# Performance work log

Measured on AMD Instinct MI355X. Metric: run time of the kernel, lower is better.

The kernel has to match this reference:

```python
import jax, jax.numpy as jnp
import numpy as np

CUTOFF = 5.0  # Angstrom contact cutoff for atom interaction mask
N, L, ATOMS, D, H = 1, 64, 14, 128, 64
M = L * ATOMS  # 896 atoms


def atom_interaction_mask_batch(pos14, ppi_code, cutoff=CUTOFF):
    # pos14: (N, L, 14, 3), ppi_code: (N, L) -> mask (N, L*14, L*14)
    n, l = ppi_code.shape
    pos = pos14.reshape(n, l * ATOMS, 3)
    d2 = jnp.sum((pos[:, :, None, :] - pos[:, None, :, :]) ** 2, axis=-1)  # (N,M,M)
    codes = jnp.repeat(ppi_code, ATOMS, axis=1)  # (N,M)
    cross_chain = codes[:, :, None] != codes[:, None, :]
    return (d2 < cutoff * cutoff) & cross_chain


def _edge_feats(feats, W1, b1, mask):
    # Decompose fc_1(concat(f_i, f_j)) = f_i @ W1[:, :D].T + f_j @ W1[:, D:].T + b1
    # so the (N,M,M,2D) concat tensor is never materialized.
    d = feats.shape[-1]
    hi = feats @ W1[:, :d].T  # (N,M,H)
    hj = feats @ W1[:, d:].T  # (N,M,H)
    e = hi[:, :, None, :] + hj[:, None, :, :] + b1  # (N,M,M,H)
    return jnp.where(mask[..., None], e, 0.0)


def setup_inputs() -> dict:
    key = jax.random.key(0)
    ks = jax.random.split(key, 8)
    feats_wt = jax.random.normal(ks[0], (N, M, D), dtype=jnp.float32)
    feats_mut = jax.random.normal(ks[1], (N, M, D), dtype=jnp.float32)
    # scale positions so the 5A cutoff yields a sparse, realistic contact mask
    pos14_wt = jax.random.normal(ks[2], (N, L, ATOMS, 3), dtype=jnp.float32) * 10.0
    pos14_mut = pos14_wt + jax.random.normal(ks[3], (N, L, ATOMS, 3), dtype=jnp.float32) * 0.5
    ppi_code_wt = jax.random.randint(ks[4], (N, L), 0, 2)
    ppi_code_mut = ppi_code_wt
    # fc_1: Linear(2D -> H), fc_2: Linear(H -> 1), torch layout W:(out,in)
    W1 = jax.random.normal(ks[5], (H, 2 * D), dtype=jnp.float32) / np.sqrt(2 * D)
    b1 = jnp.zeros((H,), dtype=jnp.float32)
    W2 = jax.random.normal(ks[6], (1, H), dtype=jnp.float32) / np.sqrt(H)
    b2 = jnp.zeros((1,), dtype=jnp.float32)
    return dict(feats_wt=feats_wt, feats_mut=feats_mut, pos14_wt=pos14_wt,
                pos14_mut=pos14_mut, ppi_code_wt=ppi_code_wt,
                ppi_code_mut=ppi_code_mut, W1=W1, b1=b1, W2=W2, b2=b2)


def reference(feats_wt, feats_mut, pos14_wt, pos14_mut, ppi_code_wt,
              ppi_code_mut, W1, b1, W2, b2):
    mask_wt = atom_interaction_mask_batch(pos14_wt, ppi_code_wt)
    mask_mut = atom_interaction_mask_batch(pos14_mut, ppi_code_mut)
    e_wt = _edge_feats(feats_wt, W1, b1, mask_wt)    # (N,M,M,H)
    e_mut = _edge_feats(feats_mut, W1, b1, mask_mut)  # (N,M,M,H)
    diff = e_mut - e_wt
    n = diff.shape[0]
    # (n, l1, 14, l2, 14, H) -> sum over residues l1, l2 -> (n, 14, 14, H)
    blocks = diff.reshape(n, L, ATOMS, L, ATOMS, H).sum(axis=(1, 3))
    out = blocks @ W2.T + b2  # (n,14,14,1)
    return out.reshape(n, -1)  # (n, 196)
```

## Files before the change

kernel.cpp:

```cpp
#include <hip/hip_runtime.h>

#define LRES   64
#define ATOMS  14
#define M      896
#define DF     128
#define HF     64
#define CUT2   25.0f

#define U_OFF    0
#define V_OFF    128
#define SB_OFF   256
#define SIW_OFF  320
#define SJW_OFF  (320 + 896)
#define SIM_OFF  (320 + 2*896)
#define SJM_OFF  (320 + 3*896)
#define PART_OFF (320 + 4*896)

__global__ void k_prep_uv(const float* __restrict__ W1, const float* __restrict__ b1,
                          const float* __restrict__ W2, float* __restrict__ ws) {
    int t = threadIdx.x;
    float s = 0.f;
    #pragma unroll
    for (int h = 0; h < HF; ++h) s += W2[h] * W1[h * (2 * DF) + t];
    ws[t] = s;
    if (t == 0) {
        float sb = 0.f;
        #pragma unroll
        for (int h = 0; h < HF; ++h) sb += W2[h] * b1[h];
        ws[SB_OFF] = sb;
    }
}

__global__ void k_prep_s(const float* __restrict__ feats_wt,
                         const float* __restrict__ feats_mut,
                         float* __restrict__ ws) {
    int i = blockIdx.x;
    int t = threadIdx.x;
    const float* u = ws + U_OFF;
    const float* v = ws + V_OFF;
    float fw0 = feats_wt[i * DF + t],  fw1 = feats_wt[i * DF + 64 + t];
    float fm0 = feats_mut[i * DF + t], fm1 = feats_mut[i * DF + 64 + t];
    float u0 = u[t], u1 = u[64 + t], v0 = v[t], v1 = v[64 + t];
    float siw = fw0 * u0 + fw1 * u1;
    float sjw = fw0 * v0 + fw1 * v1;
    float sim = fm0 * u0 + fm1 * u1;
    float sjm = fm0 * v0 + fm1 * v1;
    #pragma unroll
    for (int off = 32; off > 0; off >>= 1) {
        siw += __shfl_down(siw, off);
        sjw += __shfl_down(sjw, off);
        sim += __shfl_down(sim, off);
        sjm += __shfl_down(sjm, off);
    }
    if (t == 0) {
        ws[SIW_OFF + i] = siw;
        ws[SJW_OFF + i] = sjw;
        ws[SIM_OFF + i] = sim;
        ws[SJM_OFF + i] = sjm;
    }
}

__global__ void k_pairs(const float* __restrict__ pos_wt,
                        const float* __restrict__ pos_mut,
                        const int* __restrict__ ppi_wt,
                        const int* __restrict__ ppi_mut,
                        float* __restrict__ ws) {
    int i = blockIdx.x;
    int t = threadIdx.x;
    __shared__ float acc[16][14];

    float pwx = pos_wt[i * 3 + 0], pwy = pos_wt[i * 3 + 1], pwz = pos_wt[i * 3 + 2];
    float pmx = pos_mut[i * 3 + 0], pmy = pos_mut[i * 3 + 1], pmz = pos_mut[i * 3 + 2];
    int cw_i = ppi_wt[i / ATOMS];
    int cm_i = ppi_mut[i / ATOMS];
    float sb = ws[SB_OFF];
    float base_w = ws[SIW_OFF + i] + sb;
    float base_m = ws[SIM_OFF + i] + sb;
    const float* sjw = ws + SJW_OFF;
    const float* sjm = ws + SJM_OFF;

    if (t < 14 * 16) {
        int a2 = t % ATOMS;
        int k  = t / ATOMS;
        float c = 0.f;
        for (int l2 = k; l2 < LRES; l2 += 16) {
            int j = l2 * ATOMS + a2;
            if (ppi_wt[l2] != cw_i) {
                float dx = pwx - pos_wt[j * 3 + 0];
                float dy = pwy - pos_wt[j * 3 + 1];
                float dz = pwz - pos_wt[j * 3 + 2];
                float d2 = dx * dx + dy * dy + dz * dz;
                if (d2 < CUT2) c -= base_w + sjw[j];
            }
            if (ppi_mut[l2] != cm_i) {
                float dx = pmx - pos_mut[j * 3 + 0];
                float dy = pmy - pos_mut[j * 3 + 1];
                float dz = pmz - pos_mut[j * 3 + 2];
                float d2 = dx * dx + dy * dy + dz * dz;
                if (d2 < CUT2) c += base_m + sjm[j];
            }
        }
        acc[k][a2] = c;
    }
    __syncthreads();
    if (t < ATOMS) {
        float s = 0.f;
        #pragma unroll
        for (int k = 0; k < 16; ++k) s += acc[k][t];
        ws[PART_OFF + i * ATOMS + t] = s;
    }
}

__global__ void k_final(const float* __restrict__ b2, const float* __restrict__ ws,
                        float* __restrict__ out) {
    int t = threadIdx.x;
    if (t < ATOMS * ATOMS) {
        int a1 = t / ATOMS, a2 = t % ATOMS;
        float s = 0.f;
        #pragma unroll
        for (int l1 = 0; l1 < LRES; ++l1)
            s += ws[PART_OFF + (l1 * ATOMS + a1) * ATOMS + a2];
        out[t] = s + b2[0];
    }
}

extern "C" void kernel_launch(void* const* d_in, const int* in_sizes, int n_in,
                              void* d_out, int out_size, void* d_ws, size_t ws_size,
                              hipStream_t stream) {
    const float* feats_wt  = (const float*)d_in[0];
    const float* feats_mut = (const float*)d_in[1];
    const float* pos_wt    = (const float*)d_in[2];
    const float* pos_mut   = (const float*)d_in[3];
    const int*   ppi_wt    = (const int*)d_in[4];
    const int*   ppi_mut   = (const int*)d_in[5];
    const float* W1        = (const float*)d_in[6];
    const float* b1        = (const float*)d_in[7];
    const float* W2        = (const float*)d_in[8];
    const float* b2        = (const float*)d_in[9];
    float* out = (float*)d_out;
    float* ws  = (float*)d_ws;

    k_prep_uv<<<1, 256, 0, stream>>>(W1, b1, W2, ws);
    k_prep_s<<<M, 64, 0, stream>>>(feats_wt, feats_mut, ws);
    k_pairs<<<M, 256, 0, stream>>>(pos_wt, pos_mut, ppi_wt, ppi_mut, ws);
    k_final<<<1, 256, 0, stream>>>(b2, ws, out);
}
```

Before: 18.37 us.

## Fuse all four kernels into one per-output-block kernel using contact counts

Replaces the four-kernel pipeline (prep u/v, prep per-atom scalars, pair scan, final reduce) with a single kernel of 196 blocks, one per output atom pair (a1,a2). Each block recomputes the folded W2·W1 vectors in shared memory and, for each residue l1, counts cutoff-satisfying cross-chain contacts for the row atom and the column atom. It then multiplies those counts by per-atom projected features, so no workspace round trips or extra launches are needed. The cost is redundant recomputation of u/v and the feature dot products in every block, and fewer blocks (196) than before.

```diff
diff --git a/kernel.cpp b/kernel.cpp
--- a/kernel.cpp
+++ b/kernel.cpp
@@ -7,120 +7,112 @@
 #define HF     64
 #define CUT2   25.0f
 
-#define U_OFF    0
-#define V_OFF    128
-#define SB_OFF   256
-#define SIW_OFF  320
-#define SJW_OFF  (320 + 896)
-#define SIM_OFF  (320 + 2*896)
-#define SJM_OFF  (320 + 3*896)
-#define PART_OFF (320 + 4*896)
+__global__ __launch_bounds__(256) void k_fused(
+    const float* __restrict__ feats_wt, const float* __restrict__ feats_mut,
+    const float* __restrict__ pos_wt,   const float* __restrict__ pos_mut,
+    const int* __restrict__ ppi_wt,     const int* __restrict__ ppi_mut,
+    const float* __restrict__ W1, const float* __restrict__ b1,
+    const float* __restrict__ W2, const float* __restrict__ b2,
+    float* __restrict__ out)
+{
+    const int b  = blockIdx.x;
+    const int a1 = b / ATOMS, a2 = b % ATOMS;
+    const int t  = threadIdx.x;
+    const int l1 = t >> 2;
+    const int c  = t & 3;
 
-__global__ void k_prep_uv(const float* __restrict__ W1, const float* __restrict__ b1,
-                          const float* __restrict__ W2, float* __restrict__ ws) {
-    int t = threadIdx.x;
-    float s = 0.f;
-    #pragma unroll
-    for (int h = 0; h < HF; ++h) s += W2[h] * W1[h * (2 * DF) + t];
-    ws[t] = s;
-    if (t == 0) {
-        float sb = 0.f;
-        #pragma unroll
-        for (int h = 0; h < HF; ++h) sb += W2[h] * b1[h];
-        ws[SB_OFF] = sb;
-    }
-}
+    __shared__ float u[DF], v[DF];
+    __shared__ float sbs;
+    __shared__ float part[LRES];
 
-__global__ void k_prep_s(const float* __restrict__ feats_wt,
-                         const float* __restrict__ feats_mut,
-                         float* __restrict__ ws) {
-    int i = blockIdx.x;
-    int t = threadIdx.x;
-    const float* u = ws + U_OFF;
-    const float* v = ws + V_OFF;
-    float fw0 = feats_wt[i * DF + t],  fw1 = feats_wt[i * DF + 64 + t];
-    float fm0 = feats_mut[i * DF + t], fm1 = feats_mut[i * DF + 64 + t];
-    float u0 = u[t], u1 = u[64 + t], v0 = v[t], v1 = v[64 + t];
-    float siw = fw0 * u0 + fw1 * u1;
-    float sjw = fw0 * v0 + fw1 * v1;
-    float sim = fm0 * u0 + fm1 * u1;
-    float sjm = fm0 * v0 + fm1 * v1;
-    #pragma unroll
-    for (int off = 32; off > 0; off >>= 1) {
-        siw += __shfl_down(siw, off);
-        sjw += __shfl_down(sjw, off);
-        sim += __shfl_down(sim, off);
-        sjm += __shfl_down(sjm, off);
+    {
+        const int d = t & 127;
+        const float* col = W1 + ((t < 128) ? d : (DF + d));
+        float s = 0.f;
+        #pragma unroll 8
+        for (int h = 0; h < HF; ++h) s += W2[h] * col[h * (2 * DF)];
+        if (t < 128) u[d] = s; else v[d] = s;
     }
     if (t == 0) {
-        ws[SIW_OFF + i] = siw;
-        ws[SJW_OFF + i] = sjw;
-        ws[SIM_OFF + i] = sim;
-        ws[SJM_OFF + i] = sjm;
+        float s = 0.f;
+        #pragma unroll
+        for (int h = 0; h < HF; ++h) s += W2[h] * b1[h];
+        sbs = s;
     }
-}
 
-__global__ void k_pairs(const float* __restrict__ pos_wt,
-                        const float* __restrict__ pos_mut,
-                        const int* __restrict__ ppi_wt,
-                        const int* __restrict__ ppi_mut,
-                        float* __restrict__ ws) {
-    int i = blockIdx.x;
-    int t = threadIdx.x;
-    __shared__ float acc[16][14];
+    const int i_row = l1 * ATOMS + a1;
+    const int j_col = l1 * ATOMS + a2;
+    const float rwx = pos_wt [i_row*3], rwy = pos_wt [i_row*3+1], rwz = pos_wt [i_row*3+2];
+    const float rmx = pos_mut[i_row*3], rmy = pos_mut[i_row*3+1], rmz = pos_mut[i_row*3+2];
+    const float cwx = pos_wt [j_col*3], cwy = pos_wt [j_col*3+1], cwz = pos_wt [j_col*3+2];
+    const float cmx = pos_mut[j_col*3], cmy = pos_mut[j_col*3+1], cmz = pos_mut[j_col*3+2];
+    const int codew = ppi_wt[l1], codem = ppi_mut[l1];
 
-    float pwx = pos_wt[i * 3 + 0], pwy = pos_wt[i * 3 + 1], pwz = pos_wt[i * 3 + 2];
-    float pmx = pos_mut[i * 3 + 0], pmy = pos_mut[i * 3 + 1], pmz = pos_mut[i * 3 + 2];
-    int cw_i = ppi_wt[i / ATOMS];
-    int cm_i = ppi_mut[i / ATOMS];
-    float sb = ws[SB_OFF];
-    float base_w = ws[SIW_OFF + i] + sb;
-    float base_m = ws[SIM_OFF + i] + sb;
-    const float* sjw = ws + SJW_OFF;
-    const float* sjm = ws + SJM_OFF;
+    int cw_r = 0, cm_r = 0, cw_c = 0, cm_c = 0;
+    for (int l2 = c; l2 < LRES; l2 += 4) {
+        const int jw = l2 * ATOMS + a2;
+        const int iw = l2 * ATOMS + a1;
+        if (ppi_wt[l2] != codew) {
+            float dx = rwx - pos_wt[jw*3], dy = rwy - pos_wt[jw*3+1], dz = rwz - pos_wt[jw*3+2];
+            if (dx*dx + dy*dy + dz*dz < CUT2) ++cw_r;
+            dx = cwx - pos_wt[iw*3]; dy = cwy - pos_wt[iw*3+1]; dz = cwz - pos_wt[iw*3+2];
+            if (dx*dx + dy*dy + dz*dz < CUT2) ++cw_c;
+        }
+        if (ppi_mut[l2] != codem) {
+            float dx = rmx - pos_mut[jw*3], dy = rmy - pos_mut[jw*3+1], dz = rmz - pos_mut[jw*3+2];
+            if (dx*dx + dy*dy + dz*dz < CUT2) ++cm_r;
+            dx = cmx - pos_mut[iw*3]; dy = cmy - pos_mut[iw*3+1]; dz = cmz - pos_mut[iw*3+2];
+            if (dx*dx + dy*dy + dz*dz < CUT2) ++cm_c;
+        }
+    }
 
-    if (t < 14 * 16) {
-        int a2 = t % ATOMS;
-        int k  = t / ATOMS;
-        float c = 0.f;
-        for (int l2 = k; l2 < LRES; l2 += 16) {
-            int j = l2 * ATOMS + a2;
-            if (ppi_wt[l2] != cw_i) {
-                float dx = pwx - pos_wt[j * 3 + 0];
-                float dy = pwy - pos_wt[j * 3 + 1];
-                float dz = pwz - pos_wt[j * 3 + 2];
-                float d2 = dx * dx + dy * dy + dz * dz;
-                if (d2 < CUT2) c -= base_w + sjw[j];
-            }
-            if (ppi_mut[l2] != cm_i) {
-                float dx = pmx - pos_mut[j * 3 + 0];
-                float dy = pmy - pos_mut[j * 3 + 1];
-                float dz = pmz - pos_mut[j * 3 + 2];
-                float d2 = dx * dx + dy * dy + dz * dz;
-                if (d2 < CUT2) c += base_m + sjm[j];
-            }
+    __syncthreads();
+    float si_w = 0.f, si_m = 0.f, sj_w = 0.f, sj_m = 0.f;
+    {
+        const float4* fw_r = (const float4*)(feats_wt  + i_row * DF);
+        const float4* fm_r = (const float4*)(feats_mut + i_row * DF);
+        const float4* fw_c = (const float4*)(feats_wt  + j_col * DF);
+        const float4* fm_c = (const float4*)(feats_mut + j_col * DF);
+        const float4* u4 = (const float4*)u;
+        const float4* v4 = (const float4*)v;
+        #pragma unroll
+        for (int q = c * 8; q < c * 8 + 8; ++q) {
+            const float4 uu = u4[q], vv = v4[q];
+            float4 a = fw_r[q];
+            si_w += a.x*uu.x + a.y*uu.y + a.z*uu.z + a.w*uu.w;
+            a = fm_r[q];
+            si_m += a.x*uu.x + a.y*uu.y + a.z*uu.z + a.w*uu.w;
+            a = fw_c[q];
+            sj_w += a.x*vv.x + a.y*vv.y + a.z*vv.z + a.w*vv.w;
+            a = fm_c[q];
+            sj_m += a.x*vv.x + a.y*vv.y + a.z*vv.z + a.w*vv.w;
         }
-        acc[k][a2] = c;
+    }
+
+    #pragma unroll
+    for (int off = 2; off > 0; off >>= 1) {
+        si_w += __shfl_down(si_w, off, 4);
+        si_m += __shfl_down(si_m, off, 4);
+        sj_w += __shfl_down(sj_w, off, 4);
+        sj_m += __shfl_down(sj_m, off, 4);
+        cw_r += __shfl_down(cw_r, off, 4);
+        cm_r += __shfl_down(cm_r, off, 4);
+        cw_c += __shfl_down(cw_c, off, 4);
+        cm_c += __shfl_down(cm_c, off, 4);
+    }
+    if (c == 0) {
+        const float sb = sbs;
+        const float rowt = (si_m + sb) * (float)cm_r - (si_w + sb) * (float)cw_r;
+        const float colt = sj_m * (float)cm_c - sj_w * (float)cw_c;
+        part[l1] = rowt + colt;
     }
     __syncthreads();
-    if (t < ATOMS) {
+
+    if (t == 0) {
         float s = 0.f;
         #pragma unroll
-        for (int k = 0; k < 16; ++k) s += acc[k][t];
-        ws[PART_OFF + i * ATOMS + t] = s;
-    }
-}
-
-__global__ void k_final(const float* __restrict__ b2, const float* __restrict__ ws,
-                        float* __restrict__ out) {
-    int t = threadIdx.x;
-    if (t < ATOMS * ATOMS) {
-        int a1 = t / ATOMS, a2 = t % ATOMS;
-        float s = 0.f;
-        #pragma unroll
-        for (int l1 = 0; l1 < LRES; ++l1)
-            s += ws[PART_OFF + (l1 * ATOMS + a1) * ATOMS + a2];
-        out[t] = s + b2[0];
+        for (int k = 0; k < LRES; ++k) s += part[k];
+        out[b] = s + b2[0];
     }
 }
 
@@ -138,10 +130,8 @@
     const float* W2        = (const float*)d_in[8];
     const float* b2        = (const float*)d_in[9];
     float* out = (float*)d_out;
-    float* ws  = (float*)d_ws;
 
-    k_prep_uv<<<1, 256, 0, stream>>>(W1, b1, W2, ws);
-    k_prep_s<<<M, 64, 0, stream>>>(feats_wt, feats_mut, ws);
-    k_pairs<<<M, 256, 0, stream>>>(pos_wt, pos_mut, ppi_wt, ppi_mut, ws);
-    k_final<<<1, 256, 0, stream>>>(b2, ws, out);
+    k_fused<<<ATOMS * ATOMS, 256, 0, stream>>>(
+        feats_wt, feats_mut, pos_wt, pos_mut, ppi_wt, ppi_mut,
+        W1, b1, W2, b2, out);
 }
```

Measured after the change: 21.49 us. 1.17x slower.
